# Kernel optimization log

Measured on AMD Instinct MI355X. Metric: run time of the kernel, lower is better.

The kernel has to match this reference:

```python
import jax, jax.numpy as jnp
import numpy as np

B, S, D_MODEL, H = 2, 2048, 768, 12
HD = D_MODEL // H  # head_dim = 64
EPS = 1e-5


def setup_inputs() -> dict:
    key = jax.random.key(0)
    ks = jax.random.split(key, 5)
    sc = 0.02
    return {
        "x": jax.random.normal(ks[0], (B, S, D_MODEL), dtype=jnp.float32),
        "Wproj_w": jax.random.normal(ks[1], (7 * D_MODEL, D_MODEL), dtype=jnp.float32) * sc,
        "Wproj_b": jax.random.normal(ks[2], (7 * D_MODEL,), dtype=jnp.float32) * sc,
        "gn_w": jnp.ones((D_MODEL,), dtype=jnp.float32),
        "gn_b": jnp.zeros((D_MODEL,), dtype=jnp.float32),
        "out_w": jax.random.normal(ks[3], (D_MODEL, D_MODEL), dtype=jnp.float32) * sc,
        "out_b": jax.random.normal(ks[4], (D_MODEL,), dtype=jnp.float32) * sc,
    }


def _time_swiglu(qkv):
    # qkv: [B, S, 7, H, D]
    q1, k1, q2, k2, q3, k3, v = [qkv[:, :, i] for i in range(7)]
    a1 = jnp.einsum('bthd,bshd->bhts', q1, k1)  # [B,H,S,S], raw scores, no softmax
    a2 = jnp.einsum('bthd,bshd->bhts', q2, k2)
    a3 = jnp.einsum('bthd,bshd->bhts', q3, k3)
    t1 = jax.nn.silu(jnp.einsum('bhts,bshd->bthd', a1, v))
    t2 = jnp.einsum('bhts,bshd->bthd', a2, v)
    return jnp.einsum('bhts,bshd->bthd', a3, t1 * t2)  # [B,S,H,D]


def _group_norm(ctx, gn_w, gn_b):
    # ctx: [B, S, D_MODEL]; torch applies GroupNorm(H, D_MODEL) over (B, C=D_MODEL, L=S)
    g = ctx.reshape(B, S, H, HD)
    mean = jnp.mean(g, axis=(1, 3), keepdims=True)          # per (batch, group) over (S, HD)
    var = jnp.var(g, axis=(1, 3), keepdims=True)
    g = (g - mean) * jax.lax.rsqrt(var + EPS)
    g = g.reshape(B, S, D_MODEL)
    return g * gn_w + gn_b


def reference(x, Wproj_w, Wproj_b, gn_w, gn_b, out_w, out_b):
    qkv = x @ Wproj_w.T + Wproj_b                  # [B,S,7*D_MODEL]
    qkv = qkv.reshape(B, S, 7, H, HD)
    ctx = _time_swiglu(qkv).reshape(B, S, D_MODEL)  # [B,S,D_MODEL]
    ctx = _group_norm(ctx, gn_w, gn_b)
    return ctx @ out_w.T + out_b
```

## Files before the change

kernel.cpp:

```cpp
#include <hip/hip_runtime.h>
#include <hip/hip_bf16.h>
#include <stdint.h>

typedef short short8 __attribute__((ext_vector_type(8)));
typedef float f32x4 __attribute__((ext_vector_type(4)));
typedef float f32x16 __attribute__((ext_vector_type(16)));
typedef unsigned short u16x4 __attribute__((ext_vector_type(4)));
typedef unsigned uint4v __attribute__((ext_vector_type(4)));

#define MFMA16 __builtin_amdgcn_mfma_f32_16x16x32_bf16
#define MFMA32 __builtin_amdgcn_mfma_f32_32x32x16_bf16

typedef unsigned int __attribute__((address_space(1))) as1_u32;
typedef unsigned int __attribute__((address_space(3))) as3_u32;
#define GLOAD16(gsrc, ldst) \
  __builtin_amdgcn_global_load_lds((const as1_u32*)(gsrc), (as3_u32*)(ldst), 16, 0, 0)

__device__ __forceinline__ unsigned short f2bf(float f) {
  __hip_bfloat16 h = __float2bfloat16(f);
  return *(unsigned short*)&h;
}
__device__ __forceinline__ unsigned pk2(float lo, float hi) {
  return ((unsigned)f2bf(hi) << 16) | (unsigned)f2bf(lo);
}
__device__ __forceinline__ void plswap(unsigned &a, unsigned &b) {
  asm volatile("v_permlane32_swap_b32 %0, %1" : "+v"(a), "+v"(b));
}

__device__ __forceinline__ short8 pv_frag(const f32x16* acc, int kc2) {
  int n = kc2 >> 1, c = kc2 & 1;
  int o0 = 2 * c, o1 = 2 * c + 1;
  unsigned x0 = pk2(acc[n][o0 * 4 + 0], acc[n][o0 * 4 + 1]);
  unsigned x1 = pk2(acc[n][o0 * 4 + 2], acc[n][o0 * 4 + 3]);
  unsigned y0 = pk2(acc[n][o1 * 4 + 0], acc[n][o1 * 4 + 1]);
  unsigned y1 = pk2(acc[n][o1 * 4 + 2], acc[n][o1 * 4 + 3]);
  plswap(x0, y0);
  plswap(x1, y1);
  uint4v fu; fu.x = x0; fu.y = x1; fu.z = y0; fu.w = y1;
  return __builtin_bit_cast(short8, fu);
}

__global__ __launch_bounds__(256) void cvt_bf16_4(const float* __restrict__ in,
                                                  unsigned short* __restrict__ out,
                                                  int n) {
  int i = (blockIdx.x * 256 + threadIdx.x) * 4;
  if (i >= n) return;
  f32x4 v = *(const f32x4*)(in + i);
  u16x4 o;
  o.x = f2bf(v.x); o.y = f2bf(v.y); o.z = f2bf(v.z); o.w = f2bf(v.w);
  *(u16x4*)(out + i) = o;
}

__global__ __launch_bounds__(256) void transp64(const unsigned short* __restrict__ src,
                                                int stride, int off,
                                                unsigned short* __restrict__ dst) {
  __shared__ __align__(16) unsigned short t[64 * 64];
  const int tid = threadIdx.x;
  const int tt = blockIdx.x, bh = blockIdx.y;
  const int b = bh / 12, h = bh % 12;
  const unsigned short* sbase = src + (size_t)(b * 2048 + tt * 64) * stride + h * 64 + off;
  for (int it = 0; it < 2; ++it) {
    int slot = it * 256 + tid, s = slot >> 3, j = slot & 7;
    short8 v = *(const short8*)(sbase + (size_t)s * stride + j * 8);
    int phys = (s + 8 * j) & 63;
    for (int e = 0; e < 8; ++e)
      t[(j * 8 + e) * 64 + phys] = ((unsigned short*)&v)[e];
  }
  __syncthreads();
  unsigned short* dbase = dst + (size_t)bh * 64 * 2048 + tt * 64;
  for (int it = 0; it < 2; ++it) {
    int slot = it * 256 + tid, d = slot >> 3, c = slot & 7;
    int pc = (c + (d >> 3)) & 7;
    short8 v = *(const short8*)(t + d * 64 + pc * 8);
    *(short8*)(dbase + (size_t)d * 2048 + c * 8) = v;
  }
}

template <bool OUT_BF16>
__global__ __launch_bounds__(256) void gemm_nt(const unsigned short* __restrict__ A,
                                               const unsigned short* __restrict__ Bm,
                                               const float* __restrict__ bias,
                                               void* __restrict__ Cout,
                                               int M, int N, int K) {
  __shared__ __align__(16) char smem[32768];
  char* As = smem;
  char* Bs = smem + 16384;
  const int tid = threadIdx.x;
  const int w = tid >> 6, l = tid & 63;
  const int wm = w >> 1, wn = w & 1;
  const int Row0 = blockIdx.y * 128, Col0 = blockIdx.x * 128;

  f32x4 z; z.x = 0.f; z.y = 0.f; z.z = 0.f; z.w = 0.f;
  f32x4 acc[4][4];
  for (int m = 0; m < 4; ++m)
    for (int n = 0; n < 4; ++n) acc[m][n] = z;

  for (int k0 = 0; k0 < K; k0 += 64) {
    for (int it = 0; it < 4; ++it) {
      int slot = it * 256 + tid;
      int row = slot >> 3, j = slot & 7;
      int gc = j ^ (row & 7);
      GLOAD16(A + (size_t)(Row0 + row) * K + k0 + gc * 8, As + slot * 16);
      GLOAD16(Bm + (size_t)(Col0 + row) * K + k0 + gc * 8, Bs + slot * 16);
    }
    __syncthreads();
    for (int kc = 0; kc < 2; ++kc) {
      int c = (l >> 4) + 4 * kc;
      short8 af[4], bf[4];
      for (int m = 0; m < 4; ++m) {
        int t = wm * 64 + m * 16 + (l & 15);
        af[m] = *(const short8*)(As + t * 128 + ((c ^ (t & 7)) * 16));
      }
      for (int n = 0; n < 4; ++n) {
        int t = wn * 64 + n * 16 + (l & 15);
        bf[n] = *(const short8*)(Bs + t * 128 + ((c ^ (t & 7)) * 16));
      }
      for (int m = 0; m < 4; ++m)
        for (int n = 0; n < 4; ++n)
          acc[m][n] = MFMA16(af[m], bf[n], acc[m][n], 0, 0, 0);
    }
    __syncthreads();
  }
  for (int n = 0; n < 4; ++n) {
    int col = Col0 + wn * 64 + n * 16 + (l & 15);
    float bv = bias[col];
    for (int m = 0; m < 4; ++m) {
      int rbase = Row0 + wm * 64 + m * 16 + (l >> 4) * 4;
      for (int r = 0; r < 4; ++r) {
        float v = acc[m][n][r] + bv;
        size_t idx = (size_t)(rbase + r) * N + col;
        if (OUT_BF16) ((unsigned short*)Cout)[idx] = f2bf(v);
        else          ((float*)Cout)[idx] = v;
      }
    }
  }
}

__global__ __launch_bounds__(512, 2) void pass1(const unsigned short* __restrict__ qkv,
                                                const unsigned short* __restrict__ vt,
                                                unsigned short* __restrict__ u) {
  __shared__ __align__(16) char smem[49152];
  const int tid = threadIdx.x, w = tid >> 6, l = tid & 63;
  const int sh = w >> 2, wi = w & 3;
  const int tidh = tid & 255;
  const int g5 = l >> 5, l31 = l & 31;
  const int tt = blockIdx.x, bh = blockIdx.y;
  const int b = bh / 12, h = bh % 12;
  char* K1s = smem + sh * 24576;
  char* K2s = K1s + 8192;
  char* Vts = K1s + 16384;

  const int tg = tt * 128 + wi * 32 + l31;
  const unsigned short* qrow = qkv + (size_t)(b * 2048 + tg) * 5376 + h * 64;
  short8 q1f[4], q2f[4];
#pragma unroll
  for (int kc = 0; kc < 4; ++kc) {
    int d = kc * 16 + g5 * 8;
    q1f[kc] = *(const short8*)(qrow + 0 * 768 + d);
    q2f[kc] = *(const short8*)(qrow + 2 * 768 + d);
  }

  f32x16 z16;
#pragma unroll
  for (int i = 0; i < 16; ++i) z16[i] = 0.f;
  f32x16 t1a[2], t2a[2];
  t1a[0] = z16; t1a[1] = z16; t2a[0] = z16; t2a[1] = z16;

  for (int si = 0; si < 16; ++si) {
    const int s0 = sh * 1024 + si * 64;
#pragma unroll
    for (int it = 0; it < 2; ++it) {
      int slot = it * 256 + tidh;
      int row = slot >> 3, j = slot & 7;
      int gc = j ^ (row & 7);
      const unsigned short* ksrc =
          qkv + (size_t)(b * 2048 + s0 + row) * 5376 + h * 64 + 768 + gc * 8;
      GLOAD16(ksrc, K1s + slot * 16);
      GLOAD16(ksrc + 2 * 768, K2s + slot * 16);
      GLOAD16(vt + (size_t)(bh * 64 + row) * 2048 + s0 + gc * 8, Vts + slot * 16);
    }
    __syncthreads();

    f32x16 a1t[2], a2t[2];
    a1t[0] = z16; a1t[1] = z16; a2t[0] = z16; a2t[1] = z16;
#pragma unroll
    for (int kc = 0; kc < 4; ++kc) {
#pragma unroll
      for (int n = 0; n < 2; ++n) {
        int srow = n * 32 + l31;
        int off = srow * 128 + (((kc * 2 + g5) ^ (l31 & 7)) * 16);
        a1t[n] = MFMA32(*(const short8*)(K1s + off), q1f[kc], a1t[n], 0, 0, 0);
        a2t[n] = MFMA32(*(const short8*)(K2s + off), q2f[kc], a2t[n], 0, 0, 0);
      }
    }

#pragma unroll
    for (int kc2 = 0; kc2 < 4; ++kc2) {
      short8 pa1 = pv_frag(a1t, kc2);
      short8 pa2 = pv_frag(a2t, kc2);
#pragma unroll
      for (int dn = 0; dn < 2; ++dn) {
        int drow = dn * 32 + l31;
        short8 vf = *(const short8*)(Vts + drow * 128 + (((kc2 * 2 + g5) ^ (l31 & 7)) * 16));
        t1a[dn] = MFMA32(pa1, vf, t1a[dn], 0, 0, 0);
        t2a[dn] = MFMA32(pa2, vf, t2a[dn], 0, 0, 0);
      }
    }
    __syncthreads();
  }

  char* comb = smem + wi * 8192;
  if (sh == 1) {
#pragma unroll
    for (int c = 0; c < 8; ++c) {
      f32x4 q;
      q.x = t1a[c >> 2][(c & 3) * 4 + 0];
      q.y = t1a[c >> 2][(c & 3) * 4 + 1];
      q.z = t1a[c >> 2][(c & 3) * 4 + 2];
      q.w = t1a[c >> 2][(c & 3) * 4 + 3];
      *(f32x4*)(comb + c * 1024 + l * 16) = q;
    }
  }
  __syncthreads();
  if (sh == 0) {
#pragma unroll
    for (int c = 0; c < 8; ++c) {
      f32x4 q = *(const f32x4*)(comb + c * 1024 + l * 16);
      t1a[c >> 2][(c & 3) * 4 + 0] += q.x;
      t1a[c >> 2][(c & 3) * 4 + 1] += q.y;
      t1a[c >> 2][(c & 3) * 4 + 2] += q.z;
      t1a[c >> 2][(c & 3) * 4 + 3] += q.w;
    }
  }
  __syncthreads();
  if (sh == 1) {
#pragma unroll
    for (int c = 0; c < 8; ++c) {
      f32x4 q;
      q.x = t2a[c >> 2][(c & 3) * 4 + 0];
      q.y = t2a[c >> 2][(c & 3) * 4 + 1];
      q.z = t2a[c >> 2][(c & 3) * 4 + 2];
      q.w = t2a[c >> 2][(c & 3) * 4 + 3];
      *(f32x4*)(comb + c * 1024 + l * 16) = q;
    }
  }
  __syncthreads();
  if (sh == 0) {
#pragma unroll
    for (int c = 0; c < 8; ++c) {
      f32x4 q = *(const f32x4*)(comb + c * 1024 + l * 16);
      t2a[c >> 2][(c & 3) * 4 + 0] += q.x;
      t2a[c >> 2][(c & 3) * 4 + 1] += q.y;
      t2a[c >> 2][(c & 3) * 4 + 2] += q.z;
      t2a[c >> 2][(c & 3) * 4 + 3] += q.w;
    }
#pragma unroll
    for (int dn = 0; dn < 2; ++dn)
#pragma unroll
      for (int r = 0; r < 16; ++r) {
        int t = tt * 128 + wi * 32 + (r & 3) + 8 * (r >> 2) + 4 * g5;
        int d = dn * 32 + l31;
        float x1 = t1a[dn][r], x2 = t2a[dn][r];
        float uu = (x1 / (1.f + expf(-x1))) * x2;
        u[(size_t)(b * 2048 + t) * 768 + h * 64 + d] = f2bf(uu);
      }
  }
}

__global__ __launch_bounds__(512, 2) void pass2(const unsigned short* __restrict__ qkv,
                                                const unsigned short* __restrict__ ut,
                                                float* __restrict__ ctx,
                                                float* __restrict__ partials) {
  __shared__ __align__(16) char smem[32768];
  const int tid = threadIdx.x, w = tid >> 6, l = tid & 63;
  const int sh = w >> 2, wi = w & 3;
  const int tidh = tid & 255;
  const int g5 = l >> 5, l31 = l & 31;
  const int tt = blockIdx.x, bh = blockIdx.y;
  const int b = bh / 12, h = bh % 12;
  char* K3s = smem + sh * 16384;
  char* Uts = K3s + 8192;

  const int tg = tt * 128 + wi * 32 + l31;
  const unsigned short* qrow = qkv + (size_t)(b * 2048 + tg) * 5376 + h * 64;
  short8 q3f[4];
#pragma unroll
  for (int kc = 0; kc < 4; ++kc)
    q3f[kc] = *(const short8*)(qrow + 4 * 768 + kc * 16 + g5 * 8);

  f32x16 z16;
#pragma unroll
  for (int i = 0; i < 16; ++i) z16[i] = 0.f;
  f32x16 ca[2];
  ca[0] = z16; ca[1] = z16;

  for (int si = 0; si < 16; ++si) {
    const int s0 = sh * 1024 + si * 64;
#pragma unroll
    for (int it = 0; it < 2; ++it) {
      int slot = it * 256 + tidh;
      int row = slot >> 3, j = slot & 7;
      int gc = j ^ (row & 7);
      GLOAD16(qkv + (size_t)(b * 2048 + s0 + row) * 5376 + h * 64 + 5 * 768 + gc * 8,
              K3s + slot * 16);
      GLOAD16(ut + (size_t)(bh * 64 + row) * 2048 + s0 + gc * 8, Uts + slot * 16);
    }
    __syncthreads();

    f32x16 a3t[2];
    a3t[0] = z16; a3t[1] = z16;
#pragma unroll
    for (int kc = 0; kc < 4; ++kc) {
#pragma unroll
      for (int n = 0; n < 2; ++n) {
        int srow = n * 32 + l31;
        int off = srow * 128 + (((kc * 2 + g5) ^ (l31 & 7)) * 16);
        a3t[n] = MFMA32(*(const short8*)(K3s + off), q3f[kc], a3t[n], 0, 0, 0);
      }
    }
#pragma unroll
    for (int kc2 = 0; kc2 < 4; ++kc2) {
      short8 pa = pv_frag(a3t, kc2);
#pragma unroll
      for (int dn = 0; dn < 2; ++dn) {
        int drow = dn * 32 + l31;
        short8 uf = *(const short8*)(Uts + drow * 128 + (((kc2 * 2 + g5) ^ (l31 & 7)) * 16));
        ca[dn] = MFMA32(pa, uf, ca[dn], 0, 0, 0);
      }
    }
    __syncthreads();
  }

  char* comb = smem + wi * 8192;
  if (sh == 1) {
#pragma unroll
    for (int c = 0; c < 8; ++c) {
      f32x4 q;
      q.x = ca[c >> 2][(c & 3) * 4 + 0];
      q.y = ca[c >> 2][(c & 3) * 4 + 1];
      q.z = ca[c >> 2][(c & 3) * 4 + 2];
      q.w = ca[c >> 2][(c & 3) * 4 + 3];
      *(f32x4*)(comb + c * 1024 + l * 16) = q;
    }
  }
  __syncthreads();
  float psum = 0.f, psum2 = 0.f;
  if (sh == 0) {
#pragma unroll
    for (int c = 0; c < 8; ++c) {
      f32x4 q = *(const f32x4*)(comb + c * 1024 + l * 16);
      ca[c >> 2][(c & 3) * 4 + 0] += q.x;
      ca[c >> 2][(c & 3) * 4 + 1] += q.y;
      ca[c >> 2][(c & 3) * 4 + 2] += q.z;
      ca[c >> 2][(c & 3) * 4 + 3] += q.w;
    }
#pragma unroll
    for (int dn = 0; dn < 2; ++dn)
#pragma unroll
      for (int r = 0; r < 16; ++r) {
        int t = tt * 128 + wi * 32 + (r & 3) + 8 * (r >> 2) + 4 * g5;
        int d = dn * 32 + l31;
        float v = ca[dn][r];
        ctx[(size_t)(b * 2048 + t) * 768 + h * 64 + d] = v;
        psum += v; psum2 += v * v;
      }
  }
  __syncthreads();

  float* red = (float*)smem;
  red[tid] = psum; red[512 + tid] = psum2;
  __syncthreads();
  for (int st = 256; st > 0; st >>= 1) {
    if (tid < st) {
      red[tid] += red[tid + st];
      red[512 + tid] += red[512 + tid + st];
    }
    __syncthreads();
  }
  if (tid == 0) {
    partials[(bh * 16 + tt) * 2] = red[0];
    partials[(bh * 16 + tt) * 2 + 1] = red[512];
  }
}

__global__ __launch_bounds__(64) void gn_finalize(const float* __restrict__ partials,
                                                  float* __restrict__ stats) {
  const int g = blockIdx.x;
  const int l = threadIdx.x;
  double s = 0.0, s2 = 0.0;
  if (l < 16) {
    s = (double)partials[(g * 16 + l) * 2];
    s2 = (double)partials[(g * 16 + l) * 2 + 1];
  }
  for (int off = 32; off > 0; off >>= 1) {
    s += __shfl_down(s, off, 64);
    s2 += __shfl_down(s2, off, 64);
  }
  if (l == 0) {
    const double N = 2048.0 * 64.0;
    double mean = s / N;
    double var = s2 / N - mean * mean;
    stats[g * 2] = (float)mean;
    stats[g * 2 + 1] = (float)(1.0 / sqrt(var + 1e-5));
  }
}

__global__ __launch_bounds__(256) void gn_apply(const float* __restrict__ ctx,
                                                const float* __restrict__ stats,
                                                const float* __restrict__ gw,
                                                const float* __restrict__ gb,
                                                unsigned short* __restrict__ outc) {
  int i = blockIdx.x * 256 + threadIdx.x;
  if (i >= 4096 * 768) return;
  int c = i % 768;
  int b = i / (2048 * 768);
  int g = b * 12 + (c >> 6);
  float v = (ctx[i] - stats[2 * g]) * stats[2 * g + 1];
  outc[i] = f2bf(v * gw[c] + gb[c]);
}

extern "C" void kernel_launch(void* const* d_in, const int* in_sizes, int n_in,
                              void* d_out, int out_size, void* d_ws, size_t ws_size,
                              hipStream_t stream) {
  const float* x   = (const float*)d_in[0];
  const float* Wpw = (const float*)d_in[1];
  const float* Wpb = (const float*)d_in[2];
  const float* gnw = (const float*)d_in[3];
  const float* gnb = (const float*)d_in[4];
  const float* ow  = (const float*)d_in[5];
  const float* ob  = (const float*)d_in[6];
  float* out = (float*)d_out;

  char* ws = (char*)d_ws;
  size_t off = 0;
  auto carve = [&](size_t bytes) {
    char* p = ws + off;
    off = (off + bytes + 255) & ~(size_t)255;
    return p;
  };
  unsigned short* xb   = (unsigned short*)carve((size_t)4096 * 768 * 2);
  unsigned short* wb   = (unsigned short*)carve((size_t)5376 * 768 * 2);
  unsigned short* owb  = (unsigned short*)carve((size_t)768 * 768 * 2);
  unsigned short* qkvb = (unsigned short*)carve((size_t)4096 * 5376 * 2);
  unsigned short* ub   = (unsigned short*)carve((size_t)4096 * 768 * 2);
  unsigned short* vtb  = (unsigned short*)carve((size_t)24 * 64 * 2048 * 2);
  unsigned short* utb  = (unsigned short*)carve((size_t)24 * 64 * 2048 * 2);
  float* ctx           = (float*)carve((size_t)4096 * 768 * 4);
  float* partials      = (float*)carve(24 * 16 * 2 * 4);
  float* stats         = (float*)carve(48 * 4);

  cvt_bf16_4<<<3072, 256, 0, stream>>>(x, xb, 4096 * 768);
  cvt_bf16_4<<<4032, 256, 0, stream>>>(Wpw, wb, 5376 * 768);
  cvt_bf16_4<<<576, 256, 0, stream>>>(ow, owb, 768 * 768);

  gemm_nt<true><<<dim3(42, 32), 256, 0, stream>>>(xb, wb, Wpb, qkvb, 4096, 5376, 768);
  transp64<<<dim3(32, 24), 256, 0, stream>>>(qkvb, 5376, 6 * 768, vtb);
  pass1<<<dim3(16, 24), 512, 0, stream>>>(qkvb, vtb, ub);
  transp64<<<dim3(32, 24), 256, 0, stream>>>(ub, 768, 0, utb);
  pass2<<<dim3(16, 24), 512, 0, stream>>>(qkvb, utb, ctx, partials);
  gn_finalize<<<24, 64, 0, stream>>>(partials, stats);
  gn_apply<<<12288, 256, 0, stream>>>(ctx, stats, gnw, gnb, xb);
  gemm_nt<false><<<dim3(6, 32), 256, 0, stream>>>(xb, owb, ob, out, 4096, 768, 768);
}
```

Measured before the change: 220.7 us.

## Prefetch next K/V tiles into registers to overlap loads with MFMA

Both attention passes stop using direct global-to-LDS loads and switch to a register-staged software pipeline. The next 64-row K/V (or K3/U) tile is loaded into registers while the MFMAs run on the current tile, then written to LDS at the start of the next iteration. The goal is to hide global load latency behind compute without adding LDS. The cost is extra VGPRs at launch bounds 512x2, which could cause spills, plus an extra LDS write pass and one more barrier per iteration.

Measured after the change: 220.6 us. About the same (-0.1%).

```diff
diff --git a/kernel.cpp b/kernel.cpp
--- a/kernel.cpp
+++ b/kernel.cpp
@@ -146,9 +146,7 @@
   const int g5 = l >> 5, l31 = l & 31;
   const int tt = blockIdx.x, bh = blockIdx.y;
   const int b = bh / 12, h = bh % 12;
-  char* K1s = smem + sh * 24576;
-  char* K2s = K1s + 8192;
-  char* Vts = K1s + 16384;
+  char* half = smem + sh * 24576;
 
   const int tg = tt * 128 + wi * 32 + l31;
   const unsigned short* qrow = qkv + (size_t)(b * 2048 + tg) * 5376 + h * 64;
@@ -166,33 +164,50 @@
   f32x16 t1a[2], t2a[2];
   t1a[0] = z16; t1a[1] = z16; t2a[0] = z16; t2a[1] = z16;
 
-  for (int si = 0; si < 16; ++si) {
-    const int s0 = sh * 1024 + si * 64;
+  uint4v st[6];
+  auto LOAD = [&](int s0) {
+#pragma unroll
+    for (int it = 0; it < 2; ++it) {
+      int slot = it * 256 + tidh, row = slot >> 3, j = slot & 7, gc = j ^ (row & 7);
+      const unsigned short* ks =
+          qkv + (size_t)(b * 2048 + s0 + row) * 5376 + h * 64 + 768 + gc * 8;
+      st[it]     = *(const uint4v*)ks;
+      st[2 + it] = *(const uint4v*)(ks + 2 * 768);
+      st[4 + it] = *(const uint4v*)(vt + (size_t)(bh * 64 + row) * 2048 + s0 + gc * 8);
+    }
+  };
+  auto WRITE = [&]() {
 #pragma unroll
     for (int it = 0; it < 2; ++it) {
       int slot = it * 256 + tidh;
-      int row = slot >> 3, j = slot & 7;
-      int gc = j ^ (row & 7);
-      const unsigned short* ksrc =
-          qkv + (size_t)(b * 2048 + s0 + row) * 5376 + h * 64 + 768 + gc * 8;
-      GLOAD16(ksrc, K1s + slot * 16);
-      GLOAD16(ksrc + 2 * 768, K2s + slot * 16);
-      GLOAD16(vt + (size_t)(bh * 64 + row) * 2048 + s0 + gc * 8, Vts + slot * 16);
-    }
-    __syncthreads();
+      *(uint4v*)(half + slot * 16)         = st[it];
+      *(uint4v*)(half + 8192 + slot * 16)  = st[2 + it];
+      *(uint4v*)(half + 16384 + slot * 16) = st[4 + it];
+    }
+  };
+
+  LOAD(sh * 1024);
+  for (int si = 0; si < 16; ++si) {
+    __syncthreads();
+    WRITE();
+    __syncthreads();
+    if (si < 15) LOAD(sh * 1024 + (si + 1) * 64);
+
+    const char* Ks0 = half;
+    const char* Ks1 = half + 8192;
+    const char* Vs  = half + 16384;
 
     f32x16 a1t[2], a2t[2];
     a1t[0] = z16; a1t[1] = z16; a2t[0] = z16; a2t[1] = z16;
 #pragma unroll
-    for (int kc = 0; kc < 4; ++kc) {
-#pragma unroll
-      for (int n = 0; n < 2; ++n) {
-        int srow = n * 32 + l31;
+    for (int kc = 0; kc < 4; ++kc)
+#pragma unroll
+      for (int sn = 0; sn < 2; ++sn) {
+        int srow = sn * 32 + l31;
         int off = srow * 128 + (((kc * 2 + g5) ^ (l31 & 7)) * 16);
-        a1t[n] = MFMA32(*(const short8*)(K1s + off), q1f[kc], a1t[n], 0, 0, 0);
-        a2t[n] = MFMA32(*(const short8*)(K2s + off), q2f[kc], a2t[n], 0, 0, 0);
-      }
-    }
+        a1t[sn] = MFMA32(*(const short8*)(Ks0 + off), q1f[kc], a1t[sn], 0, 0, 0);
+        a2t[sn] = MFMA32(*(const short8*)(Ks1 + off), q2f[kc], a2t[sn], 0, 0, 0);
+      }
 
 #pragma unroll
     for (int kc2 = 0; kc2 < 4; ++kc2) {
@@ -201,13 +216,13 @@
 #pragma unroll
       for (int dn = 0; dn < 2; ++dn) {
         int drow = dn * 32 + l31;
-        short8 vf = *(const short8*)(Vts + drow * 128 + (((kc2 * 2 + g5) ^ (l31 & 7)) * 16));
+        short8 vf = *(const short8*)(Vs + drow * 128 + (((kc2 * 2 + g5) ^ (l31 & 7)) * 16));
         t1a[dn] = MFMA32(pa1, vf, t1a[dn], 0, 0, 0);
         t2a[dn] = MFMA32(pa2, vf, t2a[dn], 0, 0, 0);
       }
     }
-    __syncthreads();
-  }
+  }
+  __syncthreads();
 
   char* comb = smem + wi * 8192;
   if (sh == 1) {
@@ -278,8 +293,7 @@
   const int g5 = l >> 5, l31 = l & 31;
   const int tt = blockIdx.x, bh = blockIdx.y;
   const int b = bh / 12, h = bh % 12;
-  char* K3s = smem + sh * 16384;
-  char* Uts = K3s + 8192;
+  char* half = smem + sh * 16384;
 
   const int tg = tt * 128 + wi * 32 + l31;
   const unsigned short* qrow = qkv + (size_t)(b * 2048 + tg) * 5376 + h * 64;
@@ -294,42 +308,57 @@
   f32x16 ca[2];
   ca[0] = z16; ca[1] = z16;
 
-  for (int si = 0; si < 16; ++si) {
-    const int s0 = sh * 1024 + si * 64;
+  uint4v st[4];
+  auto LOAD = [&](int s0) {
+#pragma unroll
+    for (int it = 0; it < 2; ++it) {
+      int slot = it * 256 + tidh, row = slot >> 3, j = slot & 7, gc = j ^ (row & 7);
+      st[it]     = *(const uint4v*)(qkv + (size_t)(b * 2048 + s0 + row) * 5376 +
+                                    h * 64 + 5 * 768 + gc * 8);
+      st[2 + it] = *(const uint4v*)(ut + (size_t)(bh * 64 + row) * 2048 + s0 + gc * 8);
+    }
+  };
+  auto WRITE = [&]() {
 #pragma unroll
     for (int it = 0; it < 2; ++it) {
       int slot = it * 256 + tidh;
-      int row = slot >> 3, j = slot & 7;
-      int gc = j ^ (row & 7);
-      GLOAD16(qkv + (size_t)(b * 2048 + s0 + row) * 5376 + h * 64 + 5 * 768 + gc * 8,
-              K3s + slot * 16);
-      GLOAD16(ut + (size_t)(bh * 64 + row) * 2048 + s0 + gc * 8, Uts + slot * 16);
-    }
-    __syncthreads();
+      *(uint4v*)(half + slot * 16)        = st[it];
+      *(uint4v*)(half + 8192 + slot * 16) = st[2 + it];
+    }
+  };
+
+  LOAD(sh * 1024);
+  for (int si = 0; si < 16; ++si) {
+    __syncthreads();
+    WRITE();
+    __syncthreads();
+    if (si < 15) LOAD(sh * 1024 + (si + 1) * 64);
+
+    const char* Ks = half;
+    const char* Us = half + 8192;
 
     f32x16 a3t[2];
     a3t[0] = z16; a3t[1] = z16;
 #pragma unroll
-    for (int kc = 0; kc < 4; ++kc) {
-#pragma unroll
-      for (int n = 0; n < 2; ++n) {
-        int srow = n * 32 + l31;
+    for (int kc = 0; kc < 4; ++kc)
+#pragma unroll
+      for (int sn = 0; sn < 2; ++sn) {
+        int srow = sn * 32 + l31;
         int off = srow * 128 + (((kc * 2 + g5) ^ (l31 & 7)) * 16);
-        a3t[n] = MFMA32(*(const short8*)(K3s + off), q3f[kc], a3t[n], 0, 0, 0);
-      }
-    }
+        a3t[sn] = MFMA32(*(const short8*)(Ks + off), q3f[kc], a3t[sn], 0, 0, 0);
+      }
 #pragma unroll
     for (int kc2 = 0; kc2 < 4; ++kc2) {
       short8 pa = pv_frag(a3t, kc2);
 #pragma unroll
       for (int dn = 0; dn < 2; ++dn) {
         int drow = dn * 32 + l31;
-        short8 uf = *(const short8*)(Uts + drow * 128 + (((kc2 * 2 + g5) ^ (l31 & 7)) * 16));
+        short8 uf = *(const short8*)(Us + drow * 128 + (((kc2 * 2 + g5) ^ (l31 & 7)) * 16));
         ca[dn] = MFMA32(pa, uf, ca[dn], 0, 0, 0);
       }
     }
-    __syncthreads();
-  }
+  }
+  __syncthreads();
 
   char* comb = smem + wi * 8192;
   if (sh == 1) {
@@ -370,10 +399,10 @@
   float* red = (float*)smem;
   red[tid] = psum; red[512 + tid] = psum2;
   __syncthreads();
-  for (int st = 256; st > 0; st >>= 1) {
-    if (tid < st) {
-      red[tid] += red[tid + st];
-      red[512 + tid] += red[512 + tid + st];
+  for (int st2 = 256; st2 > 0; st2 >>= 1) {
+    if (tid < st2) {
+      red[tid] += red[tid + st2];
+      red[512 + tid] += red[512 + tid + st2];
     }
     __syncthreads();
   }
```
